# Kernel optimization log

Hardware: AMD Instinct MI355X
Metric: run time of the kernel (lower is better)

Reference implementation:

```python
import jax, jax.numpy as jnp
import numpy as np

TEMP = 0.07
GTEMP = 1.0

def _l2n(x):
    # tf.nn.l2_normalize with default axis=None: GLOBAL normalization (matches original code)
    return x * jax.lax.rsqrt(jnp.maximum(jnp.sum(x * x), 1e-12))

def _gumbel(key, shape):
    u = jax.random.uniform(key, shape, minval=1e-20, maxval=1.0)
    return -jnp.log(-jnp.log(u))

def _gumbel_softmax(key, logits, temp, hard):
    y = jax.nn.softmax((logits + _gumbel(key, logits.shape)) / temp, axis=-1)
    if hard:
        y_hard = jax.nn.one_hot(jnp.argmax(y, axis=-1), logits.shape[-1], dtype=y.dtype)
        y = y_hard + y - jax.lax.stop_gradient(y)  # straight-through
    return y

def _cross_rep(key, feat, context):
    # feat: [B, D], context: [K, D]
    k1, k2, k3 = jax.random.split(key, 3)
    kn = context @ feat.T                       # [K, B] codebook similarity
    logits = kn.T                               # [B, K]
    assign_n = _gumbel_softmax(k1, logits, GTEMP, False)   # soft assignment [B, K]
    hard_n = _gumbel_softmax(k2, logits, GTEMP, True)      # hard assignment [B, K]
    agg_n = _l2n(assign_n @ context)            # [B, D]
    # stochastic binary threshold on the K->B heat map
    eps = jax.random.uniform(k3, kn.shape)      # uniform(-0.5,0.5)*1 + 0.5 == U(0,1)
    prob = jax.nn.sigmoid(kn)
    binary = (prob > eps).astype(feat.dtype)
    assign_k = binary + prob - jax.lax.stop_gradient(prob)  # straight-through binary
    agg_k = assign_k @ feat                      # [K, D]
    agg_k = agg_k / (jnp.sum(assign_k, axis=1, keepdims=True) + 1e-8)
    agg_k = _l2n(agg_k)
    assignment = jnp.argmax(hard_n, axis=1)      # [B]
    return assignment, agg_n, agg_k

def _info_nce(q, kpos, negs, temp):
    l_pos = jnp.sum(q * kpos, axis=1, keepdims=True)   # [N, 1]
    l_neg = q @ negs.T                                  # [N, L]
    logits = jnp.concatenate([l_pos, l_neg], axis=1) / temp
    # cross-entropy with label 0 (positive in first column)
    return jnp.mean(jax.nn.logsumexp(logits, axis=1) - logits[:, 0])

def reference(feat_1, feat_2, context_1, context_2, queue_n, queue_k):
    key = jax.random.key(42)
    kq, kc1, kc2 = jax.random.split(key, 3)
    qn = jax.lax.stop_gradient(_l2n(queue_n))
    qk = jax.lax.stop_gradient(_l2n(queue_k))
    assign_1, agg_n_1, agg_k_1 = _cross_rep(kc1, feat_1, context_1)
    assign_2, agg_n_2, agg_k_2 = _cross_rep(kc2, feat_2, context_2)
    loss_n = _info_nce(agg_n_1, agg_n_2, qn, TEMP)
    queue = jax.lax.stop_gradient(qk + 0.1 * jax.random.normal(kq, qk.shape) + qk)
    queue = _l2n(queue)
    loss_k = _info_nce(agg_k_1, jax.lax.stop_gradient(agg_k_2), queue, TEMP)
    loss = loss_n + loss_k
    return assign_1, agg_n_2, agg_k_2, loss

def setup_inputs() -> dict:
    key = jax.random.key(0)
    k1, k2, k3, k4, k5, k6 = jax.random.split(key, 6)
    B, D, K, L, Q = 4096, 256, 512, 32768, 8192
    return {
        'feat_1': jax.random.normal(k1, (B, D), dtype=jnp.float32),
        'feat_2': jax.random.normal(k2, (B, D), dtype=jnp.float32),
        'context_1': jax.random.normal(k3, (K, D), dtype=jnp.float32) * 0.05,
        'context_2': jax.random.normal(k4, (K, D), dtype=jnp.float32) * 0.05,
        'queue_n': jax.random.normal(k5, (L, D), dtype=jnp.float32),
        'queue_k': jax.random.normal(k6, (Q, D), dtype=jnp.float32),
    }
```

## Files before the change

### kernel.cpp

```cpp
#include <hip/hip_runtime.h>
#include <stdint.h>
#include <math.h>

typedef unsigned int u32;
typedef unsigned short u16;
typedef __attribute__((ext_vector_type(8))) short short8;
typedef __attribute__((ext_vector_type(4))) float f32x4;

#define BB 4096
#define DD 256
#define KK 512
#define LL 32768
#define QQ 8192

__host__ __device__ inline void tf2x32(u32 k0, u32 k1, u32 c0, u32 c1, u32& o0, u32& o1) {
  u32 ks2 = k0 ^ k1 ^ 0x1BD11BDAu;
  u32 x0 = c0 + k0, x1 = c1 + k1;
#define TF_R(r) { x0 += x1; x1 = ((x1 << (r)) | (x1 >> (32 - (r)))); x1 ^= x0; }
  TF_R(13) TF_R(15) TF_R(26) TF_R(6)
  x0 += k1; x1 += ks2 + 1u;
  TF_R(17) TF_R(29) TF_R(16) TF_R(24)
  x0 += ks2; x1 += k0 + 2u;
  TF_R(13) TF_R(15) TF_R(26) TF_R(6)
  x0 += k0; x1 += k1 + 3u;
  TF_R(17) TF_R(29) TF_R(16) TF_R(24)
  x0 += k1; x1 += ks2 + 4u;
  TF_R(13) TF_R(15) TF_R(26) TF_R(6)
  x0 += ks2; x1 += k0 + 5u;
#undef TF_R
  o0 = x0; o1 = x1;
}

__device__ inline u32 rbits32(u32 k0, u32 k1, u32 i) {
  u32 a, b;
  tf2x32(k0, k1, 0u, i, a, b);
  return a ^ b;
}

__device__ inline float u01f(u32 bits) {
  return __uint_as_float(0x3f800000u | (bits >> 9)) - 1.0f;
}

__device__ inline float gumbel_at(u32 k0, u32 k1, u32 i) {
  float f = u01f(rbits32(k0, k1, i));
  float u = fmaxf(1e-20f, f + 1e-20f);
  float l1 = (float)log((double)u);
  float l2 = (float)log((double)(-l1));
  return -l2;
}

__device__ inline float gumbel_f32(u32 k0, u32 k1, u32 i) {
  float f = u01f(rbits32(k0, k1, i));
  float u = fmaxf(1e-20f, f + 1e-20f);
  float l1 = __logf(u);
  return -__logf(-l1);
}

__device__ inline float erfinv32(float x) {
  float w = -log1pf(-x * x);
  float p;
  if (w < 5.0f) {
    w -= 2.5f;
    p = 2.81022636e-08f;
    p = fmaf(p, w, 3.43273939e-07f);
    p = fmaf(p, w, -3.5233877e-06f);
    p = fmaf(p, w, -4.39150654e-06f);
    p = fmaf(p, w, 0.00021858087f);
    p = fmaf(p, w, -0.00125372503f);
    p = fmaf(p, w, -0.00417768164f);
    p = fmaf(p, w, 0.246640727f);
    p = fmaf(p, w, 1.50140941f);
  } else {
    w = sqrtf(w) - 3.0f;
    p = -0.000200214257f;
    p = fmaf(p, w, 0.000100950558f);
    p = fmaf(p, w, 0.00134934322f);
    p = fmaf(p, w, -0.00367342844f);
    p = fmaf(p, w, 0.00573950773f);
    p = fmaf(p, w, -0.0076224613f);
    p = fmaf(p, w, 0.00943887047f);
    p = fmaf(p, w, 1.00167406f);
    p = fmaf(p, w, 2.83297682f);
  }
  return p * x;
}

__device__ inline u16 f2bf(float f) {
  u32 u = __float_as_uint(f);
  u32 r = (u + 0x7FFFu + ((u >> 16) & 1u)) >> 16;
  return (u16)r;
}

__global__ __launch_bounds__(256)
void k_sumsq(const float* __restrict__ x, int n, float* __restrict__ partial) {
  __shared__ float sm[256];
  float s = 0.0f;
  for (int i = blockIdx.x * 256 + threadIdx.x; i < n; i += gridDim.x * 256) {
    float v = x[i]; s = fmaf(v, v, s);
  }
  sm[threadIdx.x] = s; __syncthreads();
  for (int off = 128; off > 0; off >>= 1) {
    if (threadIdx.x < off) sm[threadIdx.x] += sm[threadIdx.x + off];
    __syncthreads();
  }
  if (threadIdx.x == 0) partial[blockIdx.x] = sm[0];
}

__global__ __launch_bounds__(256)
void k_stats(const float* __restrict__ qn, const float* __restrict__ qk_in,
             const float* __restrict__ partK,
             float* __restrict__ colpart, float* __restrict__ sqpart,
             u32 kqa, u32 kqb) {
  __shared__ float smc[4][256];
  __shared__ float sm[256];
  int tid = threadIdx.x, g = tid >> 6, l = tid & 63;
  int z = blockIdx.y;
  float4 ca = {0.f, 0.f, 0.f, 0.f};
  float ss = 0.0f;
  if (z == 0) {
    int base = blockIdx.x * 64;
    for (int j = base + g; j < base + 64; j += 4) {
      float4 v = *(const float4*)(qn + (size_t)j * 256 + l * 4);
      ca.x += v.x; ca.y += v.y; ca.z += v.z; ca.w += v.w;
      ss = fmaf(v.x, v.x, ss); ss = fmaf(v.y, v.y, ss);
      ss = fmaf(v.z, v.z, ss); ss = fmaf(v.w, v.w, ss);
    }
  } else {
    sm[tid] = partK[tid]; __syncthreads();
    for (int off = 128; off > 0; off >>= 1) {
      if (tid < off) sm[tid] += sm[tid + off];
      __syncthreads();
    }
    float sk = (float)(1.0 / sqrt((double)fmaxf(sm[0], 1e-12f)));
    __syncthreads();
    const float lo = -0.99999994f;
    int base = blockIdx.x * 16;
    for (int j = base + g; j < base + 16; j += 4) {
      int i0 = j * 256 + l * 4;
      float4 v = *(const float4*)(qk_in + i0);
      float vin[4] = {v.x, v.y, v.z, v.w};
      float valv[4];
#pragma unroll
      for (int e = 0; e < 4; e++) {
        float qk = vin[e] * sk;
        float f = u01f(rbits32(kqa, kqb, (u32)(i0 + e)));
        float u = fmaxf(lo, f * 2.0f + lo);
        float nv = 1.41421354f * erfinv32(u);
        float t = qk + 0.1f * nv;
        valv[e] = t + qk;
        ss = fmaf(valv[e], valv[e], ss);
      }
      ca.x += valv[0]; ca.y += valv[1]; ca.z += valv[2]; ca.w += valv[3];
    }
  }
  smc[g][l * 4 + 0] = ca.x; smc[g][l * 4 + 1] = ca.y;
  smc[g][l * 4 + 2] = ca.z; smc[g][l * 4 + 3] = ca.w;
  sm[tid] = ss; __syncthreads();
  colpart[(size_t)z * 131072 + blockIdx.x * 256 + tid] =
      (smc[0][tid] + smc[1][tid]) + (smc[2][tid] + smc[3][tid]);
  for (int off = 128; off > 0; off >>= 1) {
    if (tid < off) sm[tid] += sm[tid + off];
    __syncthreads();
  }
  if (tid == 0) sqpart[z * 512 + blockIdx.x] = sm[0];
}

__global__ __launch_bounds__(256)
void k_finalize(const float* __restrict__ colpart, const float* __restrict__ sqpart,
                float* __restrict__ csum, float* __restrict__ lscOut) {
  __shared__ float sm[256];
  int z = blockIdx.y, t = threadIdx.x;
  if (blockIdx.x < 256) {
    int d = blockIdx.x;
    const float* cp = colpart + (size_t)z * 131072;
    float a = cp[(size_t)t * 256 + d] + cp[(size_t)(t + 256) * 256 + d];
    sm[t] = a; __syncthreads();
    for (int off = 128; off > 0; off >>= 1) {
      if (t < off) sm[t] += sm[t + off];
      __syncthreads();
    }
    if (t == 0) csum[z * 256 + d] = sm[0];
  } else {
    const float* sq = sqpart + z * 512;
    float a = sq[t] + sq[t + 256];
    sm[t] = a; __syncthreads();
    for (int off = 128; off > 0; off >>= 1) {
      if (t < off) sm[t] += sm[t + off];
      __syncthreads();
    }
    if (t == 0) {
      float sr = (float)(1.0 / sqrt((double)fmaxf(sm[0], 1e-12f)));
      lscOut[z] = sr / 0.07f;
    }
  }
}

__global__ __launch_bounds__(256)
void k_pack(const float* __restrict__ f0, const float* __restrict__ f1,
            const float* __restrict__ c0, const float* __restrict__ c1,
            u16* __restrict__ featP, u16* __restrict__ ctxP) {
  int idx = blockIdx.x * 256 + threadIdx.x;
  if (idx < 2 * BB * DD) {
    int br = idx >> 20;
    int r = idx & ((1 << 20) - 1);
    int b = r >> 8, d = r & 255;
    float v = (br ? f1 : f0)[r];
    size_t dst = ((size_t)(br * 16 + (d >> 4)) * 128 + (b >> 5)) * 512 +
                 (((d & 15) | (((b >> 3) & 3) << 4)) * 8) + (b & 7);
    featP[dst] = f2bf(v);
  } else {
    int j = idx - 2 * BB * DD;
    if (j < 2 * KK * DD) {
      int br = j >> 17;
      int r = j & 131071;
      int k = r >> 8, n = r & 255;
      float v = (br ? c1 : c0)[r];
      size_t dst = ((size_t)(br * 16 + (n >> 4)) * 16 + (k >> 5)) * 512 +
                   (((n & 15) | (((k >> 3) & 3) << 4)) * 8) + (k & 7);
      ctxP[dst] = f2bf(v);
    }
  }
}

__global__ __launch_bounds__(256)
void k_gemm_nt(const float* __restrict__ A0, const float* __restrict__ A1,
               const float* __restrict__ B0, const float* __restrict__ B1,
               float* __restrict__ C, u16* __restrict__ BINP,
               u32 k3a0, u32 k3b0, u32 k3a1, u32 k3b1) {
  __shared__ float As[16][68], Bs[16][68];
  __shared__ float Ts[64][65];
  int tid = threadIdx.x;
  int tx = tid & 15, ty = tid >> 4;
  int rowBase = blockIdx.y * 64, colBase = blockIdx.x * 64;
  int br = blockIdx.z;
  const float* A = br ? A1 : A0;
  const float* Bm = br ? B1 : B0;
  u32 k3a = br ? k3a1 : k3a0, k3b = br ? k3b1 : k3b0;
  float* Cd = C + (size_t)br * BB * KK;
  u16* Bd = BINP + (size_t)br * 32 * 128 * 512;
  float c[4][4] = {};
  for (int kt = 0; kt < 256; kt += 16) {
#pragma unroll
    for (int q = 0; q < 4; q++) {
      int idx = tid + 256 * q;
      int kkx = idx & 15, rr = idx >> 4;
      As[kkx][rr] = A[(size_t)(rowBase + rr) * 256 + kt + kkx];
      Bs[kkx][rr] = Bm[(size_t)(colBase + rr) * 256 + kt + kkx];
    }
    __syncthreads();
#pragma unroll
    for (int kx = 0; kx < 16; kx++) {
      float4 a4 = *(const float4*)&As[kx][ty * 4];
      float4 b4 = *(const float4*)&Bs[kx][tx * 4];
      float av[4] = {a4.x, a4.y, a4.z, a4.w};
      float bv[4] = {b4.x, b4.y, b4.z, b4.w};
#pragma unroll
      for (int r = 0; r < 4; r++)
#pragma unroll
        for (int q = 0; q < 4; q++)
          c[r][q] = fmaf(av[r], bv[q], c[r][q]);
    }
    __syncthreads();
  }
#pragma unroll
  for (int r = 0; r < 4; r++)
#pragma unroll
    for (int q = 0; q < 4; q++) {
      Cd[(size_t)(rowBase + ty * 4 + r) * KK + colBase + tx * 4 + q] = c[r][q];
      Ts[ty * 4 + r][tx * 4 + q] = c[r][q];
    }
  __syncthreads();
#pragma unroll
  for (int p = 0; p < 16; p++) {
    int idx = p * 256 + tid;
    int kl = idx >> 6, bl = idx & 63;
    float x = Ts[bl][kl];
    float prob = 1.0f / (1.0f + expf(-x));
    int k = colBase + kl, b = rowBase + bl;
    u32 i = (u32)(k * BB + b);
    float eps = u01f(rbits32(k3a, k3b, i));
    size_t bo = ((size_t)(k >> 4) * 128 + (b >> 5)) * 512 +
                (((k & 15) | (((b >> 3) & 3) << 4)) * 8) + (b & 7);
    Bd[bo] = (prob > eps) ? (u16)0x3F80 : (u16)0;
  }
}

__global__ __launch_bounds__(256)
void k_mfma_aggn(const u16* __restrict__ YP, const u16* __restrict__ ctxP,
                 float* __restrict__ CPN) {
  int gx = blockIdx.x, s = blockIdx.y, br = blockIdx.z;
  int tid = threadIdx.x, w = tid >> 6, lane = tid & 63;
  f32x4 acc0 = {0,0,0,0}, acc1 = {0,0,0,0}, acc2 = {0,0,0,0}, acc3 = {0,0,0,0};
  const u16* Ab = YP + ((size_t)(br * 256 + gx) * 16) * 512 + lane * 8;
  const u16* Bb = ctxP + ((size_t)(br * 16) * 16) * 512 + lane * 8;
  for (int kc = 0; kc < 8; kc++) {
    int kcg = s * 8 + kc;
    short8 a = *(const short8*)(Ab + (size_t)kcg * 512);
    short8 b0 = *(const short8*)(Bb + ((size_t)(w * 4 + 0) * 16 + kcg) * 512);
    short8 b1 = *(const short8*)(Bb + ((size_t)(w * 4 + 1) * 16 + kcg) * 512);
    short8 b2 = *(const short8*)(Bb + ((size_t)(w * 4 + 2) * 16 + kcg) * 512);
    short8 b3 = *(const short8*)(Bb + ((size_t)(w * 4 + 3) * 16 + kcg) * 512);
    acc0 = __builtin_amdgcn_mfma_f32_16x16x32_bf16(a, b0, acc0, 0, 0, 0);
    acc1 = __builtin_amdgcn_mfma_f32_16x16x32_bf16(a, b1, acc1, 0, 0, 0);
    acc2 = __builtin_amdgcn_mfma_f32_16x16x32_bf16(a, b2, acc2, 0, 0, 0);
    acc3 = __builtin_amdgcn_mfma_f32_16x16x32_bf16(a, b3, acc3, 0, 0, 0);
  }
  float* dst = CPN + (size_t)(br * 2 + s) * BB * DD;
  int rbase = gx * 16 + (lane >> 4) * 4;
  int cl = lane & 15;
#pragma unroll
  for (int r = 0; r < 4; r++) {
    dst[(size_t)(rbase + r) * 256 + (w * 4 + 0) * 16 + cl] = acc0[r];
    dst[(size_t)(rbase + r) * 256 + (w * 4 + 1) * 16 + cl] = acc1[r];
    dst[(size_t)(rbase + r) * 256 + (w * 4 + 2) * 16 + cl] = acc2[r];
    dst[(size_t)(rbase + r) * 256 + (w * 4 + 3) * 16 + cl] = acc3[r];
  }
}

__global__ __launch_bounds__(256)
void k_mfma_aggk(const u16* __restrict__ BINP, const u16* __restrict__ featP,
                 float* __restrict__ CP) {
  int gx = blockIdx.x, s = blockIdx.y, br = blockIdx.z;
  int tid = threadIdx.x, w = tid >> 6, lane = tid & 63;
  f32x4 acc0 = {0,0,0,0}, acc1 = {0,0,0,0}, acc2 = {0,0,0,0}, acc3 = {0,0,0,0};
  const u16* Ab = BINP + ((size_t)(br * 32 + gx) * 128) * 512 + lane * 8;
  const u16* Bb = featP + ((size_t)(br * 16) * 128) * 512 + lane * 8;
  for (int kc = 0; kc < 8; kc++) {
    int bcg = s * 8 + kc;
    short8 a = *(const short8*)(Ab + (size_t)bcg * 512);
    short8 b0 = *(const short8*)(Bb + ((size_t)(w * 4 + 0) * 128 + bcg) * 512);
    short8 b1 = *(const short8*)(Bb + ((size_t)(w * 4 + 1) * 128 + bcg) * 512);
    short8 b2 = *(const short8*)(Bb + ((size_t)(w * 4 + 2) * 128 + bcg) * 512);
    short8 b3 = *(const short8*)(Bb + ((size_t)(w * 4 + 3) * 128 + bcg) * 512);
    acc0 = __builtin_amdgcn_mfma_f32_16x16x32_bf16(a, b0, acc0, 0, 0, 0);
    acc1 = __builtin_amdgcn_mfma_f32_16x16x32_bf16(a, b1, acc1, 0, 0, 0);
    acc2 = __builtin_amdgcn_mfma_f32_16x16x32_bf16(a, b2, acc2, 0, 0, 0);
    acc3 = __builtin_amdgcn_mfma_f32_16x16x32_bf16(a, b3, acc3, 0, 0, 0);
  }
  float* dst = CP + (size_t)(br * 16 + s) * KK * DD;
  int rbase = gx * 16 + (lane >> 4) * 4;
  int cl = lane & 15;
#pragma unroll
  for (int r = 0; r < 4; r++) {
    dst[(size_t)(rbase + r) * 256 + (w * 4 + 0) * 16 + cl] = acc0[r];
    dst[(size_t)(rbase + r) * 256 + (w * 4 + 1) * 16 + cl] = acc1[r];
    dst[(size_t)(rbase + r) * 256 + (w * 4 + 2) * 16 + cl] = acc2[r];
    dst[(size_t)(rbase + r) * 256 + (w * 4 + 3) * 16 + cl] = acc3[r];
  }
}

__global__ __launch_bounds__(256)
void k_reduce(const float* __restrict__ CPN, const float* __restrict__ CP,
              const float* __restrict__ rs2,
              float* __restrict__ N0, float* __restrict__ N1,
              float* __restrict__ K0, float* __restrict__ K1,
              float* __restrict__ sqpN, float* __restrict__ sqpK) {
  __shared__ float sq[256];
  int tid = threadIdx.x, br = blockIdx.y;
  float v;
  if (blockIdx.x < 4096) {
    int i = blockIdx.x * 256 + tid;
    const int MN = BB * DD;
    v = CPN[(size_t)(2 * br) * MN + i] + CPN[(size_t)(2 * br + 1) * MN + i];
    (br ? N1 : N0)[i] = v;
  } else {
    int i = (blockIdx.x - 4096) * 256 + tid;
    const int MN = KK * DD;
    const float* cp = CP + (size_t)br * 16 * MN;
    float s = 0.0f;
    for (int t = 0; t < 16; t++) s += cp[(size_t)t * MN + i];
    v = s / (rs2[br * KK + (i >> 8)] + 1e-8f);
    (br ? K1 : K0)[i] = v;
  }
  sq[tid] = v * v; __syncthreads();
  for (int off = 128; off > 0; off >>= 1) {
    if (tid < off) sq[tid] += sq[tid + off];
    __syncthreads();
  }
  if (tid == 0) {
    if (blockIdx.x < 4096) sqpN[br * 4096 + blockIdx.x] = sq[0];
    else sqpK[br * 512 + (blockIdx.x - 4096)] = sq[0];
  }
}

__global__ __launch_bounds__(256)
void k_scale(float* __restrict__ N0, float* __restrict__ N1,
             float* __restrict__ K0, float* __restrict__ K1,
             const float* __restrict__ sqpN, const float* __restrict__ sqpK) {
  __shared__ float sm[256];
  int tid = threadIdx.x, br = blockIdx.y;
  int isK = (blockIdx.x >= 1024);
  const float* sq = isK ? (sqpK + br * 512) : (sqpN + br * 4096);
  int np = isK ? 512 : 4096;
  float a = 0.0f;
  for (int i = tid; i < np; i += 256) a += sq[i];
  sm[tid] = a; __syncthreads();
  for (int off = 128; off > 0; off >>= 1) {
    if (tid < off) sm[tid] += sm[tid + off];
    __syncthreads();
  }
  float f = (float)(1.0 / sqrt((double)fmaxf(sm[0], 1e-12f)));
  float* data = isK ? (br ? K1 : K0) : (br ? N1 : N0);
  int xb = isK ? (blockIdx.x - 1024) : blockIdx.x;
  int i = (xb * 256 + tid) * 4;
  float4 v = *(const float4*)(data + i);
  v.x *= f; v.y *= f; v.z *= f; v.w *= f;
  *(float4*)(data + i) = v;
}

__global__ __launch_bounds__(256)
void k_softmax_assign(const float* __restrict__ T, u16* __restrict__ YP,
                      float* __restrict__ assignOut,
                      u32 g1a0, u32 g1b0, u32 g1a1, u32 g1b1, u32 g2a, u32 g2b) {
  __shared__ float smA[4], smS[4], smM2[4], smS2[4], smV[4], smV2[4];
  __shared__ int smI[4];
  int bid = blockIdx.x, tid = threadIdx.x;
  int br = bid >> 12, b = bid & 4095;
  u32 g1a = br ? g1a1 : g1a0, g1b = br ? g1b1 : g1b0;
  const float* knT = T + (size_t)br * BB * KK;
  int lane = tid & 63, wid = tid >> 6;
  int i0 = b * KK + tid, i1 = i0 + 256;
  float x0 = knT[i0], x1 = knT[i1];

  float z0 = x0 + gumbel_f32(g1a, g1b, (u32)i0);
  float z1 = x1 + gumbel_f32(g1a, g1b, (u32)i1);
  float wm = fmaxf(z0, z1);
#pragma unroll
  for (int off = 1; off < 64; off <<= 1) wm = fmaxf(wm, __shfl_xor(wm, off, 64));
  if (lane == 0) smA[wid] = wm;
  __syncthreads();
  float m = fmaxf(fmaxf(smA[0], smA[1]), fmaxf(smA[2], smA[3]));
  float e0 = expf(z0 - m), e1 = expf(z1 - m);
  float ws = e0 + e1;
#pragma unroll
  for (int off = 1; off < 64; off <<= 1) ws += __shfl_xor(ws, off, 64);
  if (lane == 0) smS[wid] = ws;
  __syncthreads();
  float s = (smS[0] + smS[1]) + (smS[2] + smS[3]);
  {
    int k0 = tid, k1 = tid + 256;
    size_t y0o = ((size_t)(br * 256 + (b >> 4)) * 16 + (k0 >> 5)) * 512 +
                 ((b & 15) | (((k0 >> 3) & 3) << 4)) * 8 + (k0 & 7);
    size_t y1o = ((size_t)(br * 256 + (b >> 4)) * 16 + (k1 >> 5)) * 512 +
                 ((b & 15) | (((k1 >> 3) & 3) << 4)) * 8 + (k1 & 7);
    YP[y0o] = f2bf(e0 / s);
    YP[y1o] = f2bf(e1 / s);
  }

  if (br == 0) {
    float wf0 = x0 + gumbel_f32(g2a, g2b, (u32)i0);
    float wf1 = x1 + gumbel_f32(g2a, g2b, (u32)i1);
    float v1, v2; int i1x;
    if (wf0 >= wf1) { v1 = wf0; i1x = tid; v2 = wf1; }
    else            { v1 = wf1; i1x = tid + 256; v2 = wf0; }
#pragma unroll
    for (int off = 1; off < 64; off <<= 1) {
      float ov1 = __shfl_xor(v1, off, 64);
      int   oi1 = __shfl_xor(i1x, off, 64);
      float ov2 = __shfl_xor(v2, off, 64);
      float n1; int ni;
      if (ov1 > v1 || (ov1 == v1 && oi1 < i1x)) { n1 = ov1; ni = oi1; v2 = fmaxf(v1, ov2); }
      else { n1 = v1; ni = i1x; v2 = fmaxf(v2, ov1 == v1 ? ov2 : ov1); }
      if (ov1 == v1 && oi1 != i1x) v2 = fmaxf(v2, ov1);
      v1 = n1; i1x = ni;
    }
    if (lane == 0) { smV[wid] = v1; smI[wid] = i1x; smV2[wid] = v2; }
    __syncthreads();
    __shared__ int needSlow;
    if (tid == 0) {
      float cv = smV[0]; int ci = smI[0]; float c2 = smV2[0];
#pragma unroll
      for (int t = 1; t < 4; t++) {
        float tv = smV[t]; int ti = smI[t]; float t2 = smV2[t];
        if (tv > cv || (tv == cv && ti < ci)) { c2 = fmaxf(cv, t2); cv = tv; ci = ti; }
        else c2 = fmaxf(c2, tv);
      }
      if (cv - c2 > 5e-5f) { assignOut[b] = (float)ci; needSlow = 0; }
      else needSlow = 1;
    }
    __syncthreads();
    if (needSlow) {
      float w0 = x0 + gumbel_at(g2a, g2b, (u32)i0);
      float w1 = x1 + gumbel_at(g2a, g2b, (u32)i1);
      float wm2 = fmaxf(w0, w1);
#pragma unroll
      for (int off = 1; off < 64; off <<= 1) wm2 = fmaxf(wm2, __shfl_xor(wm2, off, 64));
      if (lane == 0) smM2[wid] = wm2;
      __syncthreads();
      float m2 = fmaxf(fmaxf(smM2[0], smM2[1]), fmaxf(smM2[2], smM2[3]));
      float f0 = expf(w0 - m2), f1 = expf(w1 - m2);
      float ws2 = f0 + f1;
#pragma unroll
      for (int off = 1; off < 64; off <<= 1) ws2 += __shfl_xor(ws2, off, 64);
      if (lane == 0) smS2[wid] = ws2;
      __syncthreads();
      float s2 = (smS2[0] + smS2[1]) + (smS2[2] + smS2[3]);
      float y0 = f0 / s2, y1v = f1 / s2;
      float bv; int bi;
      if (y1v > y0) { bv = y1v; bi = tid + 256; } else { bv = y0; bi = tid; }
#pragma unroll
      for (int off = 1; off < 64; off <<= 1) {
        float ov = __shfl_xor(bv, off, 64);
        int oi = __shfl_xor(bi, off, 64);
        if (ov > bv || (ov == bv && oi < bi)) { bv = ov; bi = oi; }
      }
      if (lane == 0) { smV[wid] = bv; smI[wid] = bi; }
      __syncthreads();
      if (tid == 0) {
        float cv = smV[0]; int ci = smI[0];
#pragma unroll
        for (int t = 1; t < 4; t++) {
          if (smV[t] > cv || (smV[t] == cv && smI[t] < ci)) { cv = smV[t]; ci = smI[t]; }
        }
        assignOut[b] = (float)ci;
      }
    }
  }
}

__global__ __launch_bounds__(256)
void k_rowsum(const u16* __restrict__ BINP, float* __restrict__ rs2) {
  __shared__ int sm[256];
  int bid = blockIdx.x, br = bid >> 9, k = bid & 511;
  const u16* base = BINP + ((size_t)(br * 32 + (k >> 4)) * 128) * 512;
  int klane = k & 15;
  int tid = threadIdx.x;
  int cnt = 0;
#pragma unroll
  for (int p = 0; p < 2; p++) {
    int idx = p * 256 + tid;
    int bc = idx >> 2, hi = idx & 3;
    const u16* ptr = base + (size_t)bc * 512 + (klane | (hi << 4)) * 8;
    uint4 v = *(const uint4*)ptr;
    cnt += (int)((v.x >> 7) & 1) + (int)((v.x >> 23) & 1)
         + (int)((v.y >> 7) & 1) + (int)((v.y >> 23) & 1)
         + (int)((v.z >> 7) & 1) + (int)((v.z >> 23) & 1)
         + (int)((v.w >> 7) & 1) + (int)((v.w >> 23) & 1);
  }
  sm[tid] = cnt; __syncthreads();
  for (int off = 128; off > 0; off >>= 1) {
    if (tid < off) sm[tid] += sm[tid + off];
    __syncthreads();
  }
  if (tid == 0) rs2[bid] = (float)sm[0];
}

__global__ __launch_bounds__(256)
void k_loss_row(const float* __restrict__ QN, const float* __restrict__ KPN,
                const float* __restrict__ QK, const float* __restrict__ KPK,
                const float* __restrict__ csum, const float* __restrict__ lscp,
                float* __restrict__ LPN, float* __restrict__ LPK) {
  __shared__ float pt[4];
  int w = threadIdx.x >> 6, l = threadIdx.x & 63;
  int bid = blockIdx.x;
  int isK = (bid >= 1024);
  int rb = isK ? (bid - 1024) : bid;
  const float* Q  = isK ? QK : QN;
  const float* KP = isK ? KPK : KPN;
  const float* cs4 = csum + (isK ? 256 : 0);
  float Lc = isK ? (float)QQ : (float)LL;
  float lsc = lscp[isK ? 1 : 0];
  int r = rb * 4 + w;
  float4 q = *(const float4*)(Q + (size_t)r * 256 + l * 4);
  float4 kp = *(const float4*)(KP + (size_t)r * 256 + l * 4);
  float4 cs = *(const float4*)(cs4 + l * 4);
  float d1 = q.x * kp.x + q.y * kp.y + q.z * kp.z + q.w * kp.w;
  float d2 = q.x * cs.x + q.y * cs.y + q.z * cs.z + q.w * cs.w;
#pragma unroll
  for (int off = 1; off < 64; off <<= 1) {
    d1 += __shfl_xor(d1, off, 64);
    d2 += __shfl_xor(d2, off, 64);
  }
  if (l == 0) {
    float z0 = d1 / 0.07f;
    double S = (double)Lc + (double)expf(z0) + (double)(lsc * d2);
    pt[w] = (float)(log(S)) - z0;
  }
  __syncthreads();
  if (threadIdx.x == 0) {
    float v = (pt[0] + pt[1]) + (pt[2] + pt[3]);
    if (isK) LPK[rb] = v; else LPN[rb] = v;
  }
}

__global__ __launch_bounds__(256)
void k_loss_final(const float* __restrict__ LPN, int nN, float invMN,
                  const float* __restrict__ LPK, int nK, float invMK,
                  float* __restrict__ outLoss) {
  __shared__ float sm[256];
  int tid = threadIdx.x;
  float a = 0.0f;
  for (int i = tid; i < nN; i += 256) a += LPN[i];
  sm[tid] = a; __syncthreads();
  for (int off = 128; off > 0; off >>= 1) {
    if (tid < off) sm[tid] += sm[tid + off];
    __syncthreads();
  }
  float lossN = sm[0] * invMN;
  __syncthreads();
  float b = 0.0f;
  for (int i = tid; i < nK; i += 256) b += LPK[i];
  sm[tid] = b; __syncthreads();
  for (int off = 128; off > 0; off >>= 1) {
    if (tid < off) sm[tid] += sm[tid + off];
    __syncthreads();
  }
  if (tid == 0) outLoss[0] = lossN + sm[0] * invMK;
}

extern "C" void kernel_launch(void* const* d_in, const int* in_sizes, int n_in,
                              void* d_out, int out_size, void* d_ws, size_t ws_size,
                              hipStream_t stream) {
  const float* feat0 = (const float*)d_in[0];
  const float* feat1 = (const float*)d_in[1];
  const float* ctx0  = (const float*)d_in[2];
  const float* ctx1  = (const float*)d_in[3];
  const float* queue_n = (const float*)d_in[4];
  const float* queue_k = (const float*)d_in[5];

  float* W = (float*)d_ws;
  size_t o = 0;
  float* T     = W + o; o += 2 * (size_t)BB * KK;
  float* CP    = W + o; o += 32 * (size_t)KK * DD;
  float* CPN   = W + o; o += 4 * (size_t)BB * DD;
  float* AGGN1 = W + o; o += (size_t)BB * DD;
  float* AGGK1 = W + o; o += (size_t)KK * DD;
  float* RS2   = W + o; o += 2 * KK;
  float* CPS   = W + o; o += 2 * 131072;
  float* SQ2   = W + o; o += 2 * 512;
  float* CS    = W + o; o += 2 * 256;
  float* LSC   = W + o; o += 2;
  float* LPN   = W + o; o += 1024;
  float* LPK   = W + o; o += 128;
  float* PART_K = W + o; o += 256;
  float* SQPN  = W + o; o += 2 * 4096;
  float* SQPK  = W + o; o += 2 * 512;
  u16* YP    = (u16*)(W + o); o += (size_t)BB * KK;
  u16* BINP  = (u16*)(W + o); o += (size_t)BB * KK;
  u16* featP = (u16*)(W + o); o += (size_t)BB * DD;
  u16* ctxP  = (u16*)(W + o); o += (size_t)KK * DD;

  float* out = (float*)d_out;
  float* outAssign = out;
  float* outAggn2  = out + BB;
  float* outAggk2  = out + BB + (size_t)BB * DD;
  float* outLoss   = out + BB + (size_t)BB * DD + (size_t)KK * DD;

  u32 kq0, kq1, kc[2][2];
  tf2x32(0u, 42u, 0u, 0u, kq0, kq1);
  tf2x32(0u, 42u, 0u, 1u, kc[0][0], kc[0][1]);
  tf2x32(0u, 42u, 0u, 2u, kc[1][0], kc[1][1]);
  u32 sub[2][3][2];
  for (int br = 0; br < 2; br++)
    for (int t = 0; t < 3; t++)
      tf2x32(kc[br][0], kc[br][1], 0u, (u32)t, sub[br][t][0], sub[br][t][1]);

  k_sumsq<<<256, 256, 0, stream>>>(queue_k, QQ * DD, PART_K);
  k_stats<<<dim3(512, 2), 256, 0, stream>>>(queue_n, queue_k, PART_K, CPS, SQ2, kq0, kq1);
  k_finalize<<<dim3(257, 2), 256, 0, stream>>>(CPS, SQ2, CS, LSC);
  k_pack<<<(2 * BB * DD + 2 * KK * DD) / 256, 256, 0, stream>>>(
      feat0, feat1, ctx0, ctx1, featP, ctxP);

  k_gemm_nt<<<dim3(KK / 64, BB / 64, 2), 256, 0, stream>>>(
      feat0, feat1, ctx0, ctx1, T, BINP,
      sub[0][2][0], sub[0][2][1], sub[1][2][0], sub[1][2][1]);
  k_softmax_assign<<<2 * BB, 256, 0, stream>>>(T, YP, outAssign,
      sub[0][0][0], sub[0][0][1], sub[1][0][0], sub[1][0][1], sub[0][1][0], sub[0][1][1]);
  k_rowsum<<<2 * KK, 256, 0, stream>>>(BINP, RS2);
  k_mfma_aggn<<<dim3(256, 2, 2), 256, 0, stream>>>(YP, ctxP, CPN);
  k_mfma_aggk<<<dim3(32, 16, 2), 256, 0, stream>>>(BINP, featP, CP);
  k_reduce<<<dim3(4608, 2), 256, 0, stream>>>(CPN, CP, RS2, AGGN1, outAggn2,
                                              AGGK1, outAggk2, SQPN, SQPK);
  k_scale<<<dim3(1152, 2), 256, 0, stream>>>(AGGN1, outAggn2, AGGK1, outAggk2, SQPN, SQPK);

  k_loss_row<<<1152, 256, 0, stream>>>(AGGN1, outAggn2, AGGK1, outAggk2, CS, LSC, LPN, LPK);
  k_loss_final<<<1, 256, 0, stream>>>(LPN, BB / 4, 1.0f / BB, LPK, KK / 4, 1.0f / KK, outLoss);
}
```

Baseline: 176.3 us.

## Double-buffer shared tiles with register prefetch in k_gemm_nt

Restructures the fp32 NT GEMM main loop to prefetch the next K-slice from global memory into registers while computing on the current shared-memory buffer, then writes it into a second shared buffer. This halves the barriers per iteration and overlaps global load latency with FMA work. Shared memory is pooled and reused for the transpose tile so the LDS footprint stays about the same. It adds register pressure from the prefetch registers.

```diff
diff --git a/kernel.cpp b/kernel.cpp
--- a/kernel.cpp
+++ b/kernel.cpp
@@ -227,8 +227,9 @@
                const float* __restrict__ B0, const float* __restrict__ B1,
                float* __restrict__ C, u16* __restrict__ BINP,
                u32 k3a0, u32 k3b0, u32 k3a1, u32 k3b1) {
-  __shared__ float As[16][68], Bs[16][68];
-  __shared__ float Ts[64][65];
+  __shared__ float pool[4352];
+  float (*AsP)[68] = (float(*)[68])pool;
+  float (*BsP)[68] = (float(*)[68])(pool + 2176);
   int tid = threadIdx.x;
   int tx = tid & 15, ty = tid >> 4;
   int rowBase = blockIdx.y * 64, colBase = blockIdx.x * 64;
@@ -239,19 +240,36 @@
   float* Cd = C + (size_t)br * BB * KK;
   u16* Bd = BINP + (size_t)br * 32 * 128 * 512;
   float c[4][4] = {};
-  for (int kt = 0; kt < 256; kt += 16) {
-#pragma unroll
-    for (int q = 0; q < 4; q++) {
-      int idx = tid + 256 * q;
-      int kkx = idx & 15, rr = idx >> 4;
-      As[kkx][rr] = A[(size_t)(rowBase + rr) * 256 + kt + kkx];
-      Bs[kkx][rr] = Bm[(size_t)(colBase + rr) * 256 + kt + kkx];
-    }
-    __syncthreads();
+  int kkx = tid & 15;
+  float aReg[4], bReg[4];
+#pragma unroll
+  for (int q = 0; q < 4; q++) {
+    int rr = (tid >> 4) + 16 * q;
+    aReg[q] = A[(size_t)(rowBase + rr) * 256 + kkx];
+    bReg[q] = Bm[(size_t)(colBase + rr) * 256 + kkx];
+  }
+#pragma unroll
+  for (int q = 0; q < 4; q++) {
+    int rr = (tid >> 4) + 16 * q;
+    AsP[kkx][rr] = aReg[q];
+    BsP[kkx][rr] = bReg[q];
+  }
+  __syncthreads();
+  for (int t = 0; t < 16; t++) {
+    int cur = t & 1;
+    if (t < 15) {
+      int kt = (t + 1) * 16;
+#pragma unroll
+      for (int q = 0; q < 4; q++) {
+        int rr = (tid >> 4) + 16 * q;
+        aReg[q] = A[(size_t)(rowBase + rr) * 256 + kt + kkx];
+        bReg[q] = Bm[(size_t)(colBase + rr) * 256 + kt + kkx];
+      }
+    }
 #pragma unroll
     for (int kx = 0; kx < 16; kx++) {
-      float4 a4 = *(const float4*)&As[kx][ty * 4];
-      float4 b4 = *(const float4*)&Bs[kx][tx * 4];
+      float4 a4 = *(const float4*)&AsP[cur * 16 + kx][ty * 4];
+      float4 b4 = *(const float4*)&BsP[cur * 16 + kx][tx * 4];
       float av[4] = {a4.x, a4.y, a4.z, a4.w};
       float bv[4] = {b4.x, b4.y, b4.z, b4.w};
 #pragma unroll
@@ -260,8 +278,19 @@
         for (int q = 0; q < 4; q++)
           c[r][q] = fmaf(av[r], bv[q], c[r][q]);
     }
-    __syncthreads();
-  }
+    if (t < 15) {
+      int nxt = cur ^ 1;
+#pragma unroll
+      for (int q = 0; q < 4; q++) {
+        int rr = (tid >> 4) + 16 * q;
+        AsP[nxt * 16 + kkx][rr] = aReg[q];
+        BsP[nxt * 16 + kkx][rr] = bReg[q];
+      }
+      __syncthreads();
+    }
+  }
+  __syncthreads();
+  float (*Ts)[65] = (float(*)[65])pool;
 #pragma unroll
   for (int r = 0; r < 4; r++)
 #pragma unroll
```

Result: no change. 176.5 us (+0.1%).
